# Performance work log

Hardware: AMD Instinct MI355X
Metric: run time of the kernel (lower is better)

Reference implementation:

```python
import jax, jax.numpy as jnp
import numpy as np

N_WORD, N_TOPIC, N_DOC = 30000, 1000, 15000
D_WORD, D_TOPIC, D_OUT = 300, 300, 128
E = dict(ww=800000, wt=400000, wd=600000, td=300000, tt=150000)
SRC_N = dict(ww=N_WORD, wt=N_WORD, wd=N_WORD, td=N_TOPIC, tt=N_TOPIC)
DST_N = dict(ww=N_WORD, wt=N_TOPIC, wd=N_DOC, td=N_DOC, tt=N_TOPIC)


def setup_inputs() -> dict:
    key = jax.random.key(0)
    ks = iter(jax.random.split(key, 64))
    inp = {}
    inp["feat_word"] = jax.random.normal(next(ks), (N_WORD, D_WORD), jnp.float32)
    inp["feat_topic"] = jax.random.normal(next(ks), (N_TOPIC, D_TOPIC), jnp.float32)
    for et in ["ww", "wt", "wd", "td", "tt"]:
        inp[f"{et}_src"] = jax.random.randint(next(ks), (E[et],), 0, SRC_N[et], jnp.int32)
        inp[f"{et}_dst"] = jax.random.randint(next(ks), (E[et],), 0, DST_N[et], jnp.int32)
        inp[f"{et}_w"] = jax.random.uniform(next(ks), (E[et],), jnp.float32)
        din = D_WORD if et[0] == "w" else D_TOPIC
        inp[f"W_{et}"] = jax.random.normal(next(ks), (din, D_OUT), jnp.float32) / np.float32(np.sqrt(din))
        inp[f"b_{et}"] = jnp.zeros((D_OUT,), jnp.float32)
    return inp


def _mean_agg(Wh, src, dst, w, n_dst):
    # DGL fn.u_mul_e('Wh','weight','m') + fn.mean('m','h'): per-edge message
    # Wh[src] * w, mean-reduced per destination node (0 for isolated nodes).
    m = Wh[src] * w[:, None]                                   # [E, D_OUT]
    s = jax.ops.segment_sum(m, dst, num_segments=n_dst)        # [n_dst, D_OUT]
    c = jax.ops.segment_sum(jnp.ones_like(w), dst, num_segments=n_dst)
    return s / jnp.maximum(c, 1.0)[:, None]


def reference(feat_word, feat_topic,
              ww_src, ww_dst, ww_w, wt_src, wt_dst, wt_w,
              wd_src, wd_dst, wd_w, td_src, td_dst, td_w,
              tt_src, tt_dst, tt_w,
              W_ww, b_ww, W_wt, b_wt, W_wd, b_wd, W_td, b_td, W_tt, b_tt):
    # NOTE: the original forward's causal/noise branch is dead code --
    # `Wh = self.weight[etype](feat_dict[srctype])` overwrites it, so the
    # live math is a plain per-edge-type linear projection of source feats.
    Wh_ww = feat_word @ W_ww + b_ww
    Wh_wt = feat_word @ W_wt + b_wt
    Wh_wd = feat_word @ W_wd + b_wd
    Wh_td = feat_topic @ W_td + b_td
    Wh_tt = feat_topic @ W_tt + b_tt
    # multi_update_all(..., 'sum'): sum the per-etype means per dst node type.
    h_word = _mean_agg(Wh_ww, ww_src, ww_dst, ww_w, N_WORD)
    h_topic = (_mean_agg(Wh_wt, wt_src, wt_dst, wt_w, N_TOPIC)
               + _mean_agg(Wh_tt, tt_src, tt_dst, tt_w, N_TOPIC))
    h_doc = (_mean_agg(Wh_wd, wd_src, wd_dst, wd_w, N_DOC)
             + _mean_agg(Wh_td, td_src, td_dst, td_w, N_DOC))
    return (h_word, h_topic, h_doc)
```

## Files before the change

kernel.cpp:

```cpp
#include <hip/hip_runtime.h>

#define N_WORD 30000
#define N_TOPIC 1000
#define N_DOC 15000
#define DIN 300
#define KP 320
#define DOUT 128

#define E_WW 800000
#define E_WT 400000
#define E_WD 600000
#define E_TD 300000
#define E_TT 150000

#define CC_WW 0
#define CC_WT 30000
#define CC_WD 31000
#define CC_TD 46000
#define CC_TT 61000
#define NBINS 62000

#define CAP_WW 80
#define CAP_WT 544
#define CAP_WD 96
#define CAP_TD 56
#define CAP_TT 240
#define SB_WW 0
#define SB_WT (SB_WW + N_WORD * CAP_WW)
#define SB_WD (SB_WT + N_TOPIC * CAP_WT)
#define SB_TD (SB_WD + N_DOC * CAP_WD)
#define SB_TT (SB_TD + N_DOC * CAP_TD)
#define SLOT_TOTAL (SB_TT + N_TOPIC * CAP_TT)

#define CNT_BLOCKS 360
#define PREP_BLOCKS 200
#define HIST_TOTAL 4168000

#define PFX_BLOCKS 244
#define GW_BLOCKS 469
#define GT_BLOCKS 16

#define GB_TOPIC 250
#define GB_DOC 3750
#define GB_WORD 7500

using half8  = __attribute__((ext_vector_type(8))) _Float16;
using half2v = __attribute__((ext_vector_type(2))) _Float16;
using f32x4  = __attribute__((ext_vector_type(4))) float;

struct SegP {
    const int* src[5];
    const int* dst[5];
    const float* w[5];
};

struct WPtrs {
    const float* W[5];
    const float* b[5];
};

__device__ __forceinline__ void decode_grp(
    int b, int& ti, int& hx, int& dlo, int& bins, int& hb,
    int& ch, int& ne, int& cap, int& sbase)
{
    if (b < 64)       { ti=0; hx=b;     dlo=0;     bins=15000; hb=0;       ch=12500; ne=E_WW; cap=CAP_WW; sbase=SB_WW; }
    else if (b < 128) { ti=0; hx=b-64;  dlo=15000; bins=15000; hb=960000;  ch=12500; ne=E_WW; cap=CAP_WW; sbase=SB_WW; }
    else if (b < 192) { ti=1; hx=b-128; dlo=0;     bins=1000;  hb=1920000; ch=6250;  ne=E_WT; cap=CAP_WT; sbase=SB_WT; }
    else if (b < 288) { ti=2; hx=b-192; dlo=0;     bins=15000; hb=1984000; ch=6250;  ne=E_WD; cap=CAP_WD; sbase=SB_WD; }
    else if (b < 336) { ti=3; hx=b-288; dlo=0;     bins=15000; hb=3424000; ch=6250;  ne=E_TD; cap=CAP_TD; sbase=SB_TD; }
    else              { ti=4; hx=b-336; dlo=0;     bins=1000;  hb=4144000; ch=6250;  ne=E_TT; cap=CAP_TT; sbase=SB_TT; }
}

__device__ __forceinline__ void decode_pfx(
    int b, int& hb, int& bins, int& H, int& cb, int& tile)
{
    if (b < 59)       { hb=0;       bins=15000; H=64; cb=0;     tile=b; }
    else if (b < 118) { hb=960000;  bins=15000; H=64; cb=15000; tile=b-59; }
    else if (b < 122) { hb=1920000; bins=1000;  H=64; cb=30000; tile=b-118; }
    else if (b < 181) { hb=1984000; bins=15000; H=96; cb=31000; tile=b-122; }
    else if (b < 240) { hb=3424000; bins=15000; H=48; cb=46000; tile=b-181; }
    else              { hb=4144000; bins=1000;  H=24; cb=61000; tile=b-240; }
}

__global__ __launch_bounds__(1024) void prep_count(
    SegP S, int* __restrict__ hist,
    WPtrs WP, _Float16* __restrict__ Wt_word, _Float16* __restrict__ Wt_topic,
    float* __restrict__ bcat_word, float* __restrict__ bcat_topic)
{
    __shared__ int h[15000];
    if (blockIdx.x < CNT_BLOCKS) {
        int ti, hx, dlo, bins, hb, ch, ne, cap, sbase;
        decode_grp(blockIdx.x, ti, hx, dlo, bins, hb, ch, ne, cap, sbase);
        (void)cap; (void)sbase;
        for (int i = threadIdx.x; i < bins; i += 1024) h[i] = 0;
        __syncthreads();
        const int* __restrict__ dst = S.dst[ti];
        int lo = hx * ch;
        int hiE = lo + ch; if (hiE > ne) hiE = ne;
        for (int i = lo + (int)threadIdx.x; i < hiE; i += 1024) {
            int ld = dst[i] - dlo;
            if ((unsigned)ld < (unsigned)bins) atomicAdd(&h[ld], 1);
        }
        __syncthreads();
        int* __restrict__ out = hist + hb + hx * bins;
        for (int i = threadIdx.x; i < bins; i += 1024) out[i] = h[i];
    } else {
        int id = (blockIdx.x - CNT_BLOCKS) * 1024 + threadIdx.x;
        const int total = (384 + 256) * KP;
        if (id >= total) return;
        int ng = id / KP;
        int k = id - ng * KP;
        int mat, n, lng;
        _Float16* Wt;
        float* bc;
        if (ng < 384) { lng = ng; mat = lng >> 7; Wt = Wt_word; bc = bcat_word; }
        else          { lng = ng - 384; mat = 3 + (lng >> 7); Wt = Wt_topic; bc = bcat_topic; }
        n = lng & 127;
        Wt[(size_t)lng * KP + k] =
            (k < DIN) ? (_Float16)WP.W[mat][(size_t)k * DOUT + n] : (_Float16)0.f;
        if (k == 0) bc[lng] = WP.b[mat][n];
    }
}

template <int NJ>
__device__ __forceinline__ void gemm_direct(
    const float* __restrict__ A, int M,
    const _Float16* __restrict__ Wt, const float* __restrict__ bcat,
    _Float16* __restrict__ C, int Cstride, int rowBlk)
{
    const int t = threadIdx.x;
    const int lane = t & 63;
    const int w = t >> 6;
    const int lm = lane & 15;
    const int lq = lane >> 4;
    const int rowBase = rowBlk * 64;
    const int arow = rowBase + w * 16 + lm;

    f32x4 acc[NJ];
#pragma unroll
    for (int j = 0; j < NJ; ++j) acc[j] = f32x4{0.f, 0.f, 0.f, 0.f};

    for (int kb = 0; kb < KP; kb += 32) {
        const int k0 = kb + lq * 8;
        half8 af = half8{0, 0, 0, 0, 0, 0, 0, 0};
        if (arow < M) {
            const float* ap = A + (size_t)arow * DIN + k0;
            if (k0 + 8 <= DIN) {
                float4 f0 = *(const float4*)ap;
                float4 f1 = *(const float4*)(ap + 4);
                af = half8{(_Float16)f0.x, (_Float16)f0.y, (_Float16)f0.z,
                           (_Float16)f0.w, (_Float16)f1.x, (_Float16)f1.y,
                           (_Float16)f1.z, (_Float16)f1.w};
            } else if (k0 < DIN) {
#pragma unroll
                for (int j = 0; j < 8; ++j)
                    if (k0 + j < DIN) af[j] = (_Float16)ap[j];
            }
        }
#pragma unroll
        for (int jt = 0; jt < NJ; ++jt) {
            int n = jt * 16 + lm;
            half8 bf = *(const half8*)&Wt[(size_t)n * KP + k0];
            acc[jt] = __builtin_amdgcn_mfma_f32_16x16x32_f16(af, bf, acc[jt], 0, 0, 0);
        }
    }

#pragma unroll
    for (int jt = 0; jt < NJ; ++jt) {
        int col = jt * 16 + lm;
        float bias = bcat[col];
#pragma unroll
        for (int reg = 0; reg < 4; ++reg) {
            int gr = rowBase + w * 16 + lq * 4 + reg;
            if (gr < M)
                C[(size_t)gr * Cstride + col] = (_Float16)(acc[jt][reg] + bias);
        }
    }
}

__global__ __launch_bounds__(256, 4) void phaseB(
    int* __restrict__ hist, int* __restrict__ cnt,
    const float* __restrict__ Aw, const _Float16* __restrict__ Wtw,
    const float* __restrict__ bw, _Float16* __restrict__ Cw,
    const float* __restrict__ At, const _Float16* __restrict__ Wtt,
    const float* __restrict__ bt, _Float16* __restrict__ Ct)
{
    const int b = blockIdx.x;
    if (b < PFX_BLOCKS) {
        int hb, bins, H, cb, tile;
        decode_pfx(b, hb, bins, H, cb, tile);
        int g = tile * 256 + (int)threadIdx.x;
        if (g < bins) {
            int* __restrict__ p = hist + hb + g;
            int run = 0;
            for (int h0 = 0; h0 < H; h0 += 8) {
                int v[8];
#pragma unroll
                for (int j = 0; j < 8; ++j) v[j] = p[(size_t)(h0 + j) * bins];
#pragma unroll
                for (int j = 0; j < 8; ++j) {
                    p[(size_t)(h0 + j) * bins] = run;
                    run += v[j];
                }
            }
            cnt[cb + g] = run;
        }
    } else if (b < PFX_BLOCKS + GW_BLOCKS) {
        gemm_direct<24>(Aw, N_WORD, Wtw, bw, Cw, 384, b - PFX_BLOCKS);
    } else {
        gemm_direct<16>(At, N_TOPIC, Wtt, bt, Ct, 256, b - PFX_BLOCKS - GW_BLOCKS);
    }
}

__global__ __launch_bounds__(1024) void place_k(
    SegP S, const int* __restrict__ hist, unsigned int* __restrict__ slots)
{
    __shared__ int off[15000];
    int ti, hx, dlo, bins, hb, ch, ne, cap, sbase;
    decode_grp(blockIdx.x, ti, hx, dlo, bins, hb, ch, ne, cap, sbase);
    const int* __restrict__ po = hist + hb + hx * bins;
    for (int i = threadIdx.x; i < bins; i += 1024) off[i] = po[i];
    __syncthreads();
    const int* __restrict__ dst = S.dst[ti];
    const int* __restrict__ src = S.src[ti];
    const float* __restrict__ wp = S.w[ti];
    int lo = hx * ch;
    int hiE = lo + ch; if (hiE > ne) hiE = ne;
    for (int i = lo + (int)threadIdx.x; i < hiE; i += 1024) {
        int d = dst[i];
        int ld = d - dlo;
        if ((unsigned)ld < (unsigned)bins) {
            int pos = atomicAdd(&off[ld], 1);
            if (pos < cap) {
                unsigned short hw =
                    __builtin_bit_cast(unsigned short, (_Float16)wp[i]);
                slots[(size_t)sbase + (size_t)d * cap + pos] =
                    (unsigned int)src[i] | ((unsigned int)hw << 16);
            }
        }
    }
}

#define SV2(v, i) __builtin_shufflevector(v, v, i, i + 1)

__device__ __forceinline__ _Float16 wbits(unsigned int q)
{
    return __builtin_bit_cast(_Float16, (unsigned short)(q >> 16));
}

__device__ __forceinline__ void seg_mean16(
    const unsigned int* __restrict__ slots, int beg, int ce, int c,
    const _Float16* __restrict__ rowbase, int strideh, int ln, int sub,
    float a[8])
{
    half2v ac0 = half2v{0, 0}, ac1 = half2v{0, 0};
    half2v ac2 = half2v{0, 0}, ac3 = half2v{0, 0};
    int e = 0;
    for (; e + 16 <= ce; e += 16) {
        unsigned int q0 = slots[beg + e + 0 + sub];
        unsigned int q1 = slots[beg + e + 4 + sub];
        unsigned int q2 = slots[beg + e + 8 + sub];
        unsigned int q3 = slots[beg + e + 12 + sub];
        half8 v0 = *(const half8*)(rowbase + (size_t)(q0 & 0xFFFFu) * strideh + ln * 8);
        half8 v1 = *(const half8*)(rowbase + (size_t)(q1 & 0xFFFFu) * strideh + ln * 8);
        half8 v2 = *(const half8*)(rowbase + (size_t)(q2 & 0xFFFFu) * strideh + ln * 8);
        half8 v3 = *(const half8*)(rowbase + (size_t)(q3 & 0xFFFFu) * strideh + ln * 8);
        _Float16 h0 = wbits(q0), h1 = wbits(q1), h2 = wbits(q2), h3 = wbits(q3);
        half2v w0 = half2v{h0, h0}, w1 = half2v{h1, h1};
        half2v w2 = half2v{h2, h2}, w3 = half2v{h3, h3};
        ac0 += SV2(v0, 0) * w0 + SV2(v1, 0) * w1 + SV2(v2, 0) * w2 + SV2(v3, 0) * w3;
        ac1 += SV2(v0, 2) * w0 + SV2(v1, 2) * w1 + SV2(v2, 2) * w2 + SV2(v3, 2) * w3;
        ac2 += SV2(v0, 4) * w0 + SV2(v1, 4) * w1 + SV2(v2, 4) * w2 + SV2(v3, 4) * w3;
        ac3 += SV2(v0, 6) * w0 + SV2(v1, 6) * w1 + SV2(v2, 6) * w2 + SV2(v3, 6) * w3;
    }
    for (int e2 = e + sub; e2 < ce; e2 += 4) {
        unsigned int q = slots[beg + e2];
        half8 v = *(const half8*)(rowbase + (size_t)(q & 0xFFFFu) * strideh + ln * 8);
        _Float16 h = wbits(q);
        half2v wp = half2v{h, h};
        ac0 += SV2(v, 0) * wp;
        ac1 += SV2(v, 2) * wp;
        ac2 += SV2(v, 4) * wp;
        ac3 += SV2(v, 6) * wp;
    }
    a[0] = (float)ac0.x; a[1] = (float)ac0.y;
    a[2] = (float)ac1.x; a[3] = (float)ac1.y;
    a[4] = (float)ac2.x; a[5] = (float)ac2.y;
    a[6] = (float)ac3.x; a[7] = (float)ac3.y;
#pragma unroll
    for (int j = 0; j < 8; ++j) {
        a[j] += __shfl_down(a[j], 16);
        a[j] += __shfl_down(a[j], 32);
    }
    float inv = 1.0f / (float)(c > 1 ? c : 1);
#pragma unroll
    for (int j = 0; j < 8; ++j) a[j] *= inv;
}

__global__ __launch_bounds__(256) void gather_all(
    const unsigned int* __restrict__ slots, const int* __restrict__ cnt,
    const _Float16* __restrict__ Wh_word, const _Float16* __restrict__ Wh_topic,
    float* __restrict__ out_word, float* __restrict__ out_topic,
    float* __restrict__ out_doc)
{
    const int b = blockIdx.x;
    const int t = threadIdx.x;
    const int lane = t & 63;
    const int wv = t >> 6;
    const int sub = lane >> 4;
    const int ln = lane & 15;

    float a[8];
    float* outp;
    int node;

    if (b < GB_TOPIC) {
        node = b * 4 + wv;
        int c1 = cnt[CC_WT + node];
        int ce1 = c1 < CAP_WT ? c1 : CAP_WT;
        seg_mean16(slots, SB_WT + node * CAP_WT, ce1, c1, Wh_word + 128, 384, ln, sub, a);
        int c2 = cnt[CC_TT + node];
        int ce2 = c2 < CAP_TT ? c2 : CAP_TT;
        float a2[8];
        seg_mean16(slots, SB_TT + node * CAP_TT, ce2, c2, Wh_topic + 128, 256, ln, sub, a2);
#pragma unroll
        for (int j = 0; j < 8; ++j) a[j] += a2[j];
        outp = out_topic;
    } else if (b < GB_TOPIC + GB_DOC) {
        node = (b - GB_TOPIC) * 4 + wv;
        int c1 = cnt[CC_WD + node];
        int ce1 = c1 < CAP_WD ? c1 : CAP_WD;
        seg_mean16(slots, SB_WD + node * CAP_WD, ce1, c1, Wh_word + 256, 384, ln, sub, a);
        int c2 = cnt[CC_TD + node];
        int ce2 = c2 < CAP_TD ? c2 : CAP_TD;
        float a2[8];
        seg_mean16(slots, SB_TD + node * CAP_TD, ce2, c2, Wh_topic, 256, ln, sub, a2);
#pragma unroll
        for (int j = 0; j < 8; ++j) a[j] += a2[j];
        outp = out_doc;
    } else {
        node = (b - GB_TOPIC - GB_DOC) * 4 + wv;
        int c = cnt[CC_WW + node];
        int ce = c < CAP_WW ? c : CAP_WW;
        seg_mean16(slots, SB_WW + node * CAP_WW, ce, c, Wh_word, 384, ln, sub, a);
        outp = out_word;
    }

    if (sub == 0) {
        float4* o = (float4*)outp + (size_t)node * 32 + ln * 2;
        o[0] = make_float4(a[0], a[1], a[2], a[3]);
        o[1] = make_float4(a[4], a[5], a[6], a[7]);
    }
}

extern "C" void kernel_launch(void* const* d_in, const int* in_sizes, int n_in,
                              void* d_out, int out_size, void* d_ws, size_t ws_size,
                              hipStream_t stream)
{
    const float* feat_word  = (const float*)d_in[0];
    const float* feat_topic = (const float*)d_in[1];

    const int*   ww_src = (const int*)d_in[2];
    const int*   ww_dst = (const int*)d_in[3];
    const float* ww_w   = (const float*)d_in[4];
    const float* W_ww   = (const float*)d_in[5];
    const float* b_ww   = (const float*)d_in[6];

    const int*   wt_src = (const int*)d_in[7];
    const int*   wt_dst = (const int*)d_in[8];
    const float* wt_w   = (const float*)d_in[9];
    const float* W_wt   = (const float*)d_in[10];
    const float* b_wt   = (const float*)d_in[11];

    const int*   wd_src = (const int*)d_in[12];
    const int*   wd_dst = (const int*)d_in[13];
    const float* wd_w   = (const float*)d_in[14];
    const float* W_wd   = (const float*)d_in[15];
    const float* b_wd   = (const float*)d_in[16];

    const int*   td_src = (const int*)d_in[17];
    const int*   td_dst = (const int*)d_in[18];
    const float* td_w   = (const float*)d_in[19];
    const float* W_td   = (const float*)d_in[20];
    const float* b_td   = (const float*)d_in[21];

    const int*   tt_src = (const int*)d_in[22];
    const int*   tt_dst = (const int*)d_in[23];
    const float* tt_w   = (const float*)d_in[24];
    const float* W_tt   = (const float*)d_in[25];
    const float* b_tt   = (const float*)d_in[26];

    char* wsb = (char*)d_ws;
    size_t off = 0;
    _Float16* Wh_word  = (_Float16*)(wsb + off); off += (size_t)N_WORD * 384 * 2;
    _Float16* Wh_topic = (_Float16*)(wsb + off); off += (size_t)N_TOPIC * 256 * 2;
    _Float16* Wt_word  = (_Float16*)(wsb + off); off += (size_t)384 * KP * 2;
    _Float16* Wt_topic = (_Float16*)(wsb + off); off += (size_t)256 * KP * 2;
    float* bcat_word   = (float*)(wsb + off);    off += 384 * 4;
    float* bcat_topic  = (float*)(wsb + off);    off += 256 * 4;
    unsigned int* slots = (unsigned int*)(wsb + off); off += (size_t)SLOT_TOTAL * 4;
    int* cnt_all       = (int*)(wsb + off);      off += (size_t)NBINS * 4;
    int* hist          = (int*)(wsb + off);      off += (size_t)HIST_TOTAL * 4;

    float* out_word  = (float*)d_out;
    float* out_topic = out_word + (size_t)N_WORD * DOUT;
    float* out_doc   = out_topic + (size_t)N_TOPIC * DOUT;

    SegP S;
    S.src[0] = ww_src; S.dst[0] = ww_dst; S.w[0] = ww_w;
    S.src[1] = wt_src; S.dst[1] = wt_dst; S.w[1] = wt_w;
    S.src[2] = wd_src; S.dst[2] = wd_dst; S.w[2] = wd_w;
    S.src[3] = td_src; S.dst[3] = td_dst; S.w[3] = td_w;
    S.src[4] = tt_src; S.dst[4] = tt_dst; S.w[4] = tt_w;

    WPtrs WP;
    WP.W[0] = W_ww; WP.W[1] = W_wt; WP.W[2] = W_wd; WP.W[3] = W_td; WP.W[4] = W_tt;
    WP.b[0] = b_ww; WP.b[1] = b_wt; WP.b[2] = b_wd; WP.b[3] = b_td; WP.b[4] = b_tt;

    prep_count<<<CNT_BLOCKS + PREP_BLOCKS, 1024, 0, stream>>>(
        S, hist, WP, Wt_word, Wt_topic, bcat_word, bcat_topic);
    phaseB<<<PFX_BLOCKS + GW_BLOCKS + GT_BLOCKS, 256, 0, stream>>>(
        hist, cnt_all,
        feat_word, Wt_word, bcat_word, Wh_word,
        feat_topic, Wt_topic, bcat_topic, Wh_topic);
    place_k<<<CNT_BLOCKS, 1024, 0, stream>>>(S, hist, slots);
    gather_all<<<GB_TOPIC + GB_DOC + GB_WORD, 256, 0, stream>>>(
        slots, cnt_all, Wh_word, Wh_topic, out_word, out_topic, out_doc);

    (void)in_sizes; (void)n_in; (void)ws_size;
}
```

Before: 325.4 us.

## Pre-convert features to padded fp16 and hold A fragments in registers

The fp32-to-fp16 conversion of the word and topic features moves into the first kernel, which writes padded fp16 copies into the slots buffer. The second kernel then no longer converts on the fly. The GEMM loads all ten A fragments into registers up front, and launch bounds drop to 2 blocks per SM to leave room for the extra registers. This removes repeated conversion and strided fp32 loads from the GEMM, at the cost of an extra write and read of about 19 MB of fp16 features and lower occupancy.

```diff
diff --git a/kernel.cpp b/kernel.cpp
--- a/kernel.cpp
+++ b/kernel.cpp
@@ -33,8 +33,12 @@
 #define SLOT_TOTAL (SB_TT + N_TOPIC * CAP_TT)
 
 #define CNT_BLOCKS 360
-#define PREP_BLOCKS 200
 #define HIST_TOTAL 4168000
+
+#define CVT_W_CHUNKS 1200000
+#define CVT_T_CHUNKS 40000
+#define CVT_BLOCKS 1211
+#define PREPW_BLOCKS 200
 
 #define PFX_BLOCKS 244
 #define GW_BLOCKS 469
@@ -85,12 +89,15 @@
 __global__ __launch_bounds__(1024) void prep_count(
     SegP S, int* __restrict__ hist,
     WPtrs WP, _Float16* __restrict__ Wt_word, _Float16* __restrict__ Wt_topic,
-    float* __restrict__ bcat_word, float* __restrict__ bcat_topic)
+    float* __restrict__ bcat_word, float* __restrict__ bcat_topic,
+    const float* __restrict__ feat_word, const float* __restrict__ feat_topic,
+    _Float16* __restrict__ A16w, _Float16* __restrict__ A16t)
 {
     __shared__ int h[15000];
-    if (blockIdx.x < CNT_BLOCKS) {
+    const int b = blockIdx.x;
+    if (b < CNT_BLOCKS) {
         int ti, hx, dlo, bins, hb, ch, ne, cap, sbase;
-        decode_grp(blockIdx.x, ti, hx, dlo, bins, hb, ch, ne, cap, sbase);
+        decode_grp(b, ti, hx, dlo, bins, hb, ch, ne, cap, sbase);
         (void)cap; (void)sbase;
         for (int i = threadIdx.x; i < bins; i += 1024) h[i] = 0;
         __syncthreads();
@@ -104,8 +111,31 @@
         __syncthreads();
         int* __restrict__ out = hist + hb + hx * bins;
         for (int i = threadIdx.x; i < bins; i += 1024) out[i] = h[i];
+    } else if (b < CNT_BLOCKS + CVT_BLOCKS) {
+        int c = (b - CNT_BLOCKS) * 1024 + (int)threadIdx.x;
+        if (c >= CVT_W_CHUNKS + CVT_T_CHUNKS) return;
+        const float* src;
+        _Float16* dstp;
+        int row, k8;
+        if (c < CVT_W_CHUNKS) { row = c / 40; k8 = c - row * 40; src = feat_word; dstp = A16w; }
+        else { c -= CVT_W_CHUNKS; row = c / 40; k8 = c - row * 40; src = feat_topic; dstp = A16t; }
+        int k = k8 * 8;
+        const float* ap = src + (size_t)row * DIN + k;
+        half8 hv = half8{0, 0, 0, 0, 0, 0, 0, 0};
+        if (k + 8 <= DIN) {
+            float4 f0 = *(const float4*)ap;
+            float4 f1 = *(const float4*)(ap + 4);
+            hv = half8{(_Float16)f0.x, (_Float16)f0.y, (_Float16)f0.z,
+                       (_Float16)f0.w, (_Float16)f1.x, (_Float16)f1.y,
+                       (_Float16)f1.z, (_Float16)f1.w};
+        } else if (k < DIN) {
+#pragma unroll
+            for (int j = 0; j < 8; ++j)
+                if (k + j < DIN) hv[j] = (_Float16)ap[j];
+        }
+        *(half8*)&dstp[(size_t)row * KP + k] = hv;
     } else {
-        int id = (blockIdx.x - CNT_BLOCKS) * 1024 + threadIdx.x;
+        int id = (b - CNT_BLOCKS - CVT_BLOCKS) * 1024 + (int)threadIdx.x;
         const int total = (384 + 256) * KP;
         if (id >= total) return;
         int ng = id / KP;
@@ -123,8 +153,8 @@
 }
 
 template <int NJ>
-__device__ __forceinline__ void gemm_direct(
-    const float* __restrict__ A, int M,
+__device__ __forceinline__ void gemm16(
+    const _Float16* __restrict__ A16, int M,
     const _Float16* __restrict__ Wt, const float* __restrict__ bcat,
     _Float16* __restrict__ C, int Cstride, int rowBlk)
 {
@@ -136,32 +166,27 @@
     const int rowBase = rowBlk * 64;
     const int arow = rowBase + w * 16 + lm;
 
+    half8 afv[10];
+    if (arow < M) {
+        const _Float16* ap = A16 + (size_t)arow * KP + lq * 8;
+#pragma unroll
+        for (int s = 0; s < 10; ++s) afv[s] = *(const half8*)(ap + s * 32);
+    } else {
+#pragma unroll
+        for (int s = 0; s < 10; ++s) afv[s] = half8{0, 0, 0, 0, 0, 0, 0, 0};
+    }
+
     f32x4 acc[NJ];
 #pragma unroll
     for (int j = 0; j < NJ; ++j) acc[j] = f32x4{0.f, 0.f, 0.f, 0.f};
 
-    for (int kb = 0; kb < KP; kb += 32) {
-        const int k0 = kb + lq * 8;
-        half8 af = half8{0, 0, 0, 0, 0, 0, 0, 0};
-        if (arow < M) {
-            const float* ap = A + (size_t)arow * DIN + k0;
-            if (k0 + 8 <= DIN) {
-                float4 f0 = *(const float4*)ap;
-                float4 f1 = *(const float4*)(ap + 4);
-                af = half8{(_Float16)f0.x, (_Float16)f0.y, (_Float16)f0.z,
-                           (_Float16)f0.w, (_Float16)f1.x, (_Float16)f1.y,
-                           (_Float16)f1.z, (_Float16)f1.w};
-            } else if (k0 < DIN) {
-#pragma unroll
-                for (int j = 0; j < 8; ++j)
-                    if (k0 + j < DIN) af[j] = (_Float16)ap[j];
-            }
-        }
+#pragma unroll
+    for (int s = 0; s < 10; ++s) {
+        const int k0 = s * 32 + lq * 8;
 #pragma unroll
         for (int jt = 0; jt < NJ; ++jt) {
-            int n = jt * 16 + lm;
-            half8 bf = *(const half8*)&Wt[(size_t)n * KP + k0];
-            acc[jt] = __builtin_amdgcn_mfma_f32_16x16x32_f16(af, bf, acc[jt], 0, 0, 0);
+            half8 bf = *(const half8*)&Wt[(size_t)(jt * 16 + lm) * KP + k0];
+            acc[jt] = __builtin_amdgcn_mfma_f32_16x16x32_f16(afv[s], bf, acc[jt], 0, 0, 0);
         }
     }
 
@@ -178,11 +203,11 @@
     }
 }
 
-__global__ __launch_bounds__(256, 4) void phaseB(
+__global__ __launch_bounds__(256, 2) void phaseB(
     int* __restrict__ hist, int* __restrict__ cnt,
-    const float* __restrict__ Aw, const _Float16* __restrict__ Wtw,
+    const _Float16* __restrict__ A16w, const _Float16* __restrict__ Wtw,
     const float* __restrict__ bw, _Float16* __restrict__ Cw,
-    const float* __restrict__ At, const _Float16* __restrict__ Wtt,
+    const _Float16* __restrict__ A16t, const _Float16* __restrict__ Wtt,
     const float* __restrict__ bt, _Float16* __restrict__ Ct)
 {
     const int b = blockIdx.x;
@@ -206,9 +231,9 @@
             cnt[cb + g] = run;
         }
     } else if (b < PFX_BLOCKS + GW_BLOCKS) {
-        gemm_direct<24>(Aw, N_WORD, Wtw, bw, Cw, 384, b - PFX_BLOCKS);
+        gemm16<24>(A16w, N_WORD, Wtw, bw, Cw, 384, b - PFX_BLOCKS);
     } else {
-        gemm_direct<16>(At, N_TOPIC, Wtt, bt, Ct, 256, b - PFX_BLOCKS - GW_BLOCKS);
+        gemm16<16>(A16t, N_TOPIC, Wtt, bt, Ct, 256, b - PFX_BLOCKS - GW_BLOCKS);
     }
 }
 
@@ -402,6 +427,9 @@
     int* cnt_all       = (int*)(wsb + off);      off += (size_t)NBINS * 4;
     int* hist          = (int*)(wsb + off);      off += (size_t)HIST_TOTAL * 4;
 
+    _Float16* A16w = (_Float16*)slots;
+    _Float16* A16t = A16w + (size_t)N_WORD * KP;
+
     float* out_word  = (float*)d_out;
     float* out_topic = out_word + (size_t)N_WORD * DOUT;
     float* out_doc   = out_topic + (size_t)N_TOPIC * DOUT;
@@ -417,12 +445,13 @@
     WP.W[0] = W_ww; WP.W[1] = W_wt; WP.W[2] = W_wd; WP.W[3] = W_td; WP.W[4] = W_tt;
     WP.b[0] = b_ww; WP.b[1] = b_wt; WP.b[2] = b_wd; WP.b[3] = b_td; WP.b[4] = b_tt;
 
-    prep_count<<<CNT_BLOCKS + PREP_BLOCKS, 1024, 0, stream>>>(
-        S, hist, WP, Wt_word, Wt_topic, bcat_word, bcat_topic);
+    prep_count<<<CNT_BLOCKS + CVT_BLOCKS + PREPW_BLOCKS, 1024, 0, stream>>>(
+        S, hist, WP, Wt_word, Wt_topic, bcat_word, bcat_topic,
+        feat_word, feat_topic, A16w, A16t);
     phaseB<<<PFX_BLOCKS + GW_BLOCKS + GT_BLOCKS, 256, 0, stream>>>(
         hist, cnt_all,
-        feat_word, Wt_word, bcat_word, Wh_word,
-        feat_topic, Wt_topic, bcat_topic, Wh_topic);
+        A16w, Wt_word, bcat_word, Wh_word,
+        A16t, Wt_topic, bcat_topic, Wh_topic);
     place_k<<<CNT_BLOCKS, 1024, 0, stream>>>(S, hist, slots);
     gather_all<<<GB_TOPIC + GB_DOC + GB_WORD, 256, 0, stream>>>(
         slots, cnt_all, Wh_word, Wh_topic, out_word, out_topic, out_doc);
```

After: 329.8 us. About the same (+1.4%).
